# Optimization experiments

Measured on AMD Instinct MI355X. Metric: run time of the kernel, lower is better.

Reference implementation:

```python
import jax, jax.numpy as jnp
import numpy as np

H = 1024
B = 8
T = 2048

def setup_inputs() -> dict:
    key = jax.random.key(0)
    ks = jax.random.split(key, 12)
    s = 1.0 / np.sqrt(H)
    return {
        "x": jax.random.normal(ks[0], (B, T, H), dtype=jnp.float32),
        "time_decay": jax.random.normal(ks[1], (H,), dtype=jnp.float32) * 0.1,
        "time_first": jax.random.normal(ks[2], (H,), dtype=jnp.float32) * 0.1,
        "time_mix_key": jax.random.uniform(ks[3], (1, 1, H), dtype=jnp.float32),
        "time_mix_value": jax.random.uniform(ks[4], (1, 1, H), dtype=jnp.float32),
        "time_mix_receptance": jax.random.uniform(ks[5], (1, 1, H), dtype=jnp.float32),
        "Wk": jax.random.normal(ks[6], (H, H), dtype=jnp.float32) * s,
        "Wv": jax.random.normal(ks[7], (H, H), dtype=jnp.float32) * s,
        "Wr": jax.random.normal(ks[8], (H, H), dtype=jnp.float32) * s,
        "Wo": jax.random.normal(ks[9], (H, H), dtype=jnp.float32) * s,
        "bo": jax.random.normal(ks[10], (H,), dtype=jnp.float32) * 0.01,
    }

def reference(x, time_decay, time_first, time_mix_key, time_mix_value,
              time_mix_receptance, Wk, Wv, Wr, Wo, bo):
    # time shift: shifted[:, t] = x[:, t-1], shifted[:, 0] = 0
    shifted = jnp.pad(x, ((0, 0), (1, 0), (0, 0)))[:, :-1]
    k_in = x * time_mix_key + shifted * (1.0 - time_mix_key)
    v_in = x * time_mix_value + shifted * (1.0 - time_mix_value)
    r_in = x * time_mix_receptance + shifted * (1.0 - time_mix_receptance)
    k = jnp.einsum('bth,oh->bto', k_in, Wk)
    v = jnp.einsum('bth,oh->bto', v_in, Wv)
    r = jax.nn.sigmoid(jnp.einsum('bth,oh->bto', r_in, Wr))

    td = jnp.exp(-jnp.exp(time_decay))  # (H,)

    def step(carry, kv):
        num, den = carry            # (B, H) each
        k_t, v_t = kv               # (B, H) each
        e = jnp.exp(time_first + k_t)
        out_t = (num + e * v_t) / (den + e)
        ek = jnp.exp(k_t)
        return (td * num + ek * v_t, td * den + ek), out_t

    init = (jnp.zeros((x.shape[0], x.shape[2]), x.dtype),
            jnp.zeros((x.shape[0], x.shape[2]), x.dtype))
    # scan over time: (T, B, H)
    _, wkv = jax.lax.scan(step, init, (k.transpose(1, 0, 2), v.transpose(1, 0, 2)))
    wkv = wkv.transpose(1, 0, 2)    # (B, T, H)

    return jnp.einsum('bth,oh->bto', r * wkv, Wo) + bo
```

## Files before the change

kernel.cpp:

```cpp
#include <hip/hip_runtime.h>
#include <hip/hip_bf16.h>
#include <cstdint>
#include <cstddef>

#define HH 1024
#define BB 8
#define TT 2048
#define MM (BB*TT)
#define CC 128
#define LL (TT/CC)

typedef __attribute__((ext_vector_type(8))) short bf16x8;
typedef __attribute__((ext_vector_type(8))) unsigned short u16x8;
typedef __attribute__((ext_vector_type(4))) float f32x4;

__device__ __forceinline__ unsigned short f2bf(float f) {
  union { float f; unsigned u; } v; v.f = f;
  return (unsigned short)((v.u + 0x7fffu + ((v.u >> 16) & 1u)) >> 16);
}
__device__ __forceinline__ float bf2f(unsigned short s) {
  union { float f; unsigned u; } v; v.u = ((unsigned)s) << 16;
  return v.f;
}

__device__ __forceinline__ void load_lds16(const void* g, void* l) {
  __builtin_amdgcn_global_load_lds((const __attribute__((address_space(1))) void*)g,
                                   (__attribute__((address_space(3))) void*)l,
                                   16, 0, 0);
}

__global__ __launch_bounds__(256) void conv_w(const float* __restrict__ Wk,
    const float* __restrict__ Wv, const float* __restrict__ Wr,
    const float* __restrict__ Wo, unsigned short* __restrict__ dst) {
  const int i = (blockIdx.x * 256 + threadIdx.x) * 4;
  const float* src = blockIdx.y == 0 ? Wk : blockIdx.y == 1 ? Wv : blockIdx.y == 2 ? Wr : Wo;
  const float4 v = *(const float4*)(src + i);
  ushort4 o; o.x = f2bf(v.x); o.y = f2bf(v.y); o.z = f2bf(v.z); o.w = f2bf(v.w);
  *(ushort4*)(dst + (size_t)blockIdx.y * HH * HH + i) = o;
}

__global__ __launch_bounds__(256) void mix_kernel(const float* __restrict__ x,
    const float* __restrict__ tmk, const float* __restrict__ tmv, const float* __restrict__ tmr,
    unsigned short* __restrict__ kin, unsigned short* __restrict__ vin,
    unsigned short* __restrict__ rin) {
  const int gid = blockIdx.x * 256 + threadIdx.x;
  const size_t e0 = (size_t)gid * 4;
  const int h = (int)(e0 & (HH - 1));
  const int t = (int)((e0 >> 10) & (TT - 1));
  const float4 xv = *(const float4*)(x + e0);
  float4 sv = make_float4(0.f, 0.f, 0.f, 0.f);
  if (t != 0) sv = *(const float4*)(x + e0 - HH);
  const float4 k4 = *(const float4*)(tmk + h);
  const float4 v4 = *(const float4*)(tmv + h);
  const float4 r4 = *(const float4*)(tmr + h);
  ushort4 ko, vo, ro;
  ko.x = f2bf(sv.x + k4.x * (xv.x - sv.x)); ko.y = f2bf(sv.y + k4.y * (xv.y - sv.y));
  ko.z = f2bf(sv.z + k4.z * (xv.z - sv.z)); ko.w = f2bf(sv.w + k4.w * (xv.w - sv.w));
  vo.x = f2bf(sv.x + v4.x * (xv.x - sv.x)); vo.y = f2bf(sv.y + v4.y * (xv.y - sv.y));
  vo.z = f2bf(sv.z + v4.z * (xv.z - sv.z)); vo.w = f2bf(sv.w + v4.w * (xv.w - sv.w));
  ro.x = f2bf(sv.x + r4.x * (xv.x - sv.x)); ro.y = f2bf(sv.y + r4.y * (xv.y - sv.y));
  ro.z = f2bf(sv.z + r4.z * (xv.z - sv.z)); ro.w = f2bf(sv.w + r4.w * (xv.w - sv.w));
  *(ushort4*)(kin + e0) = ko;
  *(ushort4*)(vin + e0) = vo;
  *(ushort4*)(rin + e0) = ro;
}


#define BAR()   do { asm volatile("" ::: "memory"); __builtin_amdgcn_s_barrier(); \
                     asm volatile("" ::: "memory"); } while (0)
#define VM4()   asm volatile("s_waitcnt vmcnt(4)" ::: "memory")
#define VM0()   asm volatile("s_waitcnt vmcnt(0)" ::: "memory")
#define PRIO1() __builtin_amdgcn_s_setprio(1)
#define PRIO0() __builtin_amdgcn_s_setprio(0)

__device__ __forceinline__ void stA(const unsigned short* __restrict__ Ag, int m0, int kt,
                                    unsigned short* buf, int h, int w, int rl, int scol) {
#pragma unroll
  for (int l = 0; l < 2; ++l) {
    const int row = l * 128 + h * 64 + w * 8;
    load_lds16(Ag + (size_t)(m0 + row + rl) * HH + kt + scol, buf + row * 64);
  }
}
__device__ __forceinline__ void stB(const unsigned short* __restrict__ Bg, int n0, int kt,
                                    unsigned short* buf, int h, int w, int rl, int scol) {
#pragma unroll
  for (int l = 0; l < 2; ++l) {
    const int row = (2 * (l * 2 + (w >> 2)) + h) * 32 + (w & 3) * 8;
    load_lds16(Bg + (size_t)(n0 + row + rl) * HH + kt + scol, buf + row * 64);
  }
}

template<int MH>
__device__ __forceinline__ void rdA(const unsigned short* buf, bf16x8 (&af)[4][2],
                                    int wm, int l15, int kq, int swz) {
#pragma unroll
  for (int fm = 0; fm < 4; ++fm)
#pragma unroll
    for (int kk = 0; kk < 2; ++kk)
      af[fm][kk] = *(const bf16x8*)(buf + (wm * 128 + MH * 64 + fm * 16 + l15) * 64
                                        + ((kk * 32 + kq * 8) ^ swz));
}
__device__ __forceinline__ void rdBall(const unsigned short* buf, bf16x8 (&bfr)[2][2][2],
                                       int wn, int l15, int kq, int swz) {
#pragma unroll
  for (int nh = 0; nh < 2; ++nh)
#pragma unroll
    for (int fn = 0; fn < 2; ++fn)
#pragma unroll
      for (int kk = 0; kk < 2; ++kk)
        bfr[nh][fn][kk] = *(const bf16x8*)(buf + (wn * 64 + nh * 32 + fn * 16 + l15) * 64
                                               + ((kk * 32 + kq * 8) ^ swz));
}
template<int MH>
__device__ __forceinline__ void mfma32(f32x4 (&acc)[8][4], const bf16x8 (&af)[4][2],
                                       const bf16x8 (&bfr)[2][2][2]) {
#pragma unroll
  for (int nh = 0; nh < 2; ++nh)
#pragma unroll
    for (int fn = 0; fn < 2; ++fn)
#pragma unroll
      for (int kk = 0; kk < 2; ++kk)
#pragma unroll
        for (int fm = 0; fm < 4; ++fm)
          acc[MH * 4 + fm][nh * 2 + fn] = __builtin_amdgcn_mfma_f32_16x16x32_bf16(
              bfr[nh][fn][kk], af[fm][kk], acc[MH * 4 + fm][nh * 2 + fn], 0, 0, 0);
}

__device__ __forceinline__ void gemm256(const unsigned short* __restrict__ Ag,
                                        const unsigned short* __restrict__ Bg,
                                        const int m0, const int n0,
                                        unsigned short* As, unsigned short* Bs,
                                        f32x4 (&acc)[8][4]) {
  const int tid = threadIdx.x;
  const int lane = tid & 63;
  const int w = tid >> 6;
  const int wm = w >> 2, wn = w & 3;
  const int l15 = lane & 15, kq = lane >> 4;
  const int swz = (l15 & 7) << 3;
  const int rl = lane >> 3;
  const int scol = ((lane & 7) ^ rl) * 8;
  unsigned short* const A0 = As;
  unsigned short* const A1 = As + 256 * 64;
  unsigned short* const B0 = Bs;
  unsigned short* const B1 = Bs + 256 * 64;
  bf16x8 afA[4][2], afB[4][2], bfr[2][2][2];

  stA(Ag, m0, 0, A0, 0, w, rl, scol);
  stB(Bg, n0, 0, B0, 0, w, rl, scol);
  stB(Bg, n0, 0, B0, 1, w, rl, scol);
  stA(Ag, m0, 0, A0, 1, w, rl, scol);
  stA(Ag, m0, 64, A1, 0, w, rl, scol);
  stB(Bg, n0, 64, B1, 0, w, rl, scol);
  VM4();
  BAR();
  rdA<0>(A0, afA, wm, l15, kq, swz);
  rdBall(B0, bfr, wn, l15, kq, swz);

#pragma unroll 1
  for (int i = 0; i < 8; ++i) {
    const int t1  = ((2 * i + 1) * 64) & (HH - 1);
    const int tn0 = ((2 * i + 2) * 64) & (HH - 1);
    const int tn1 = ((2 * i + 3) * 64) & (HH - 1);

    BAR();
    stB(Bg, n0, t1, B1, 1, w, rl, scol);
    stA(Ag, m0, t1, A1, 1, w, rl, scol);
    rdA<1>(A0, afB, wm, l15, kq, swz);
    PRIO1(); mfma32<0>(acc, afA, bfr); PRIO0();

    VM0();
    BAR();
    stA(Ag, m0, tn0, A0, 0, w, rl, scol);
    stB(Bg, n0, tn0, B0, 0, w, rl, scol);
    rdA<0>(A1, afA, wm, l15, kq, swz);
    PRIO1(); mfma32<1>(acc, afB, bfr); PRIO0();
    rdBall(B1, bfr, wn, l15, kq, swz);

    BAR();
    stB(Bg, n0, tn0, B0, 1, w, rl, scol);
    stA(Ag, m0, tn0, A0, 1, w, rl, scol);
    rdA<1>(A1, afB, wm, l15, kq, swz);
    PRIO1(); mfma32<0>(acc, afA, bfr); PRIO0();

    VM0();
    BAR();
    stA(Ag, m0, tn1, A1, 0, w, rl, scol);
    stB(Bg, n0, tn1, B1, 0, w, rl, scol);
    rdA<0>(A0, afA, wm, l15, kq, swz);
    PRIO1(); mfma32<1>(acc, afB, bfr); PRIO0();
    rdBall(B0, bfr, wn, l15, kq, swz);
  }
  VM0();
}

__device__ __forceinline__ void swizzle_mn256(int x, int& m0, int& n0) {
  const int wg = (x & 7) * 32 + (x >> 3);
  m0 = (wg >> 2) * 256;
  n0 = (wg & 3) * 256;
}

__global__ __launch_bounds__(512, 2) void gemm_kvr(const unsigned short* __restrict__ kin,
    const unsigned short* __restrict__ vin, const unsigned short* __restrict__ rin,
    const unsigned short* __restrict__ Wbf,
    unsigned short* __restrict__ kb, unsigned short* __restrict__ vb,
    unsigned short* __restrict__ rb) {
  __shared__ unsigned short As[2 * 256 * 64];
  __shared__ unsigned short Bs[2 * 256 * 64];
  const int z = blockIdx.y;
  const unsigned short* Ag = z == 0 ? kin : (z == 1 ? vin : rin);
  const unsigned short* Bg = Wbf + (size_t)z * HH * HH;
  unsigned short* Cg = z == 0 ? kb : (z == 1 ? vb : rb);
  int m0, n0; swizzle_mn256(blockIdx.x, m0, n0);
  f32x4 acc[8][4] = {};
  gemm256(Ag, Bg, m0, n0, As, Bs, acc);
  const int lane = threadIdx.x & 63, w = threadIdx.x >> 6;
  const int wm = w >> 2, wn = w & 3, l15 = lane & 15, lq = lane >> 4;
  const bool sig = (z == 2);
#pragma unroll
  for (int fm = 0; fm < 8; ++fm) {
    const size_t mrow = (size_t)(m0 + wm * 128 + fm * 16 + l15) * HH;
#pragma unroll
    for (int fn = 0; fn < 4; ++fn) {
      const int ncol = n0 + wn * 64 + fn * 16 + lq * 4;
      float v0 = acc[fm][fn][0], v1 = acc[fm][fn][1];
      float v2 = acc[fm][fn][2], v3 = acc[fm][fn][3];
      if (sig) {
        v0 = 1.0f / (1.0f + __expf(-v0)); v1 = 1.0f / (1.0f + __expf(-v1));
        v2 = 1.0f / (1.0f + __expf(-v2)); v3 = 1.0f / (1.0f + __expf(-v3));
      }
      ushort4 o; o.x = f2bf(v0); o.y = f2bf(v1); o.z = f2bf(v2); o.w = f2bf(v3);
      *(ushort4*)(Cg + mrow + ncol) = o;
    }
  }
}

__global__ __launch_bounds__(512, 2) void gemm_o(const unsigned short* __restrict__ Ag,
    const unsigned short* __restrict__ Bg, const float* __restrict__ bias,
    float* __restrict__ C) {
  __shared__ unsigned short As[2 * 256 * 64];
  __shared__ unsigned short Bs[2 * 256 * 64];
  int m0, n0; swizzle_mn256(blockIdx.x, m0, n0);
  f32x4 acc[8][4] = {};
  gemm256(Ag, Bg, m0, n0, As, Bs, acc);
  const int lane = threadIdx.x & 63, w = threadIdx.x >> 6;
  const int wm = w >> 2, wn = w & 3, l15 = lane & 15, lq = lane >> 4;
#pragma unroll
  for (int fm = 0; fm < 8; ++fm) {
    const size_t mrow = (size_t)(m0 + wm * 128 + fm * 16 + l15) * HH;
#pragma unroll
    for (int fn = 0; fn < 4; ++fn) {
      const int ncol = n0 + wn * 64 + fn * 16 + lq * 4;
      const float4 bv = *(const float4*)(bias + ncol);
      float4 ov;
      ov.x = acc[fm][fn][0] + bv.x; ov.y = acc[fm][fn][1] + bv.y;
      ov.z = acc[fm][fn][2] + bv.z; ov.w = acc[fm][fn][3] + bv.w;
      *(float4*)(C + mrow + ncol) = ov;
    }
  }
}

__global__ __launch_bounds__(256) void wkv_part(const unsigned short* __restrict__ k,
    const unsigned short* __restrict__ v, const float* __restrict__ tdec,
    float* __restrict__ pnum, float* __restrict__ pden) {
  const int gid = blockIdx.x * 256 + threadIdx.x;
  const int h0 = (gid & 127) * 8;
  const int b = (gid >> 7) & (BB - 1);
  const int c = gid >> 10;
  float td[8], num[8], den[8];
#pragma unroll
  for (int j = 0; j < 8; ++j) {
    td[j] = __expf(-__expf(tdec[h0 + j]));
    num[j] = 0.f; den[j] = 0.f;
  }
  size_t idx = (size_t)b * TT * HH + (size_t)(c * LL) * HH + h0;
#pragma unroll 4
  for (int i = 0; i < LL; ++i, idx += HH) {
    const u16x8 k8 = *(const u16x8*)(k + idx);
    const u16x8 v8 = *(const u16x8*)(v + idx);
#pragma unroll
    for (int j = 0; j < 8; ++j) {
      const float ek = __expf(bf2f(k8[j]));
      num[j] = td[j] * num[j] + ek * bf2f(v8[j]);
      den[j] = td[j] * den[j] + ek;
    }
  }
  const size_t o = (size_t)c * (BB * HH) + b * HH + h0;
#pragma unroll
  for (int j = 0; j < 8; ++j) { pnum[o + j] = num[j]; pden[o + j] = den[j]; }
}

__global__ __launch_bounds__(256) void wkv_scan(const float* __restrict__ tdec,
    float* __restrict__ pnum, float* __restrict__ pden) {
  const int bh = blockIdx.x * 256 + threadIdx.x;
  const int h = bh & (HH - 1);
  const float ed = __expf(tdec[h]);
  const float tdL = __expf(-ed * (float)LL);
  float num = 0.f, den = 0.f;
#pragma unroll 8
  for (int c = 0; c < CC; ++c) {
    const size_t o = (size_t)c * (BB * HH) + bh;
    const float tn = pnum[o], td_ = pden[o];
    pnum[o] = num; pden[o] = den;
    num = tdL * num + tn;
    den = tdL * den + td_;
  }
}

__global__ __launch_bounds__(256) void wkv_final(const unsigned short* __restrict__ k,
    const unsigned short* __restrict__ v, const unsigned short* __restrict__ r,
    const float* __restrict__ tdec, const float* __restrict__ tfst,
    const float* __restrict__ pnum, const float* __restrict__ pden,
    unsigned short* __restrict__ rwkv) {
  const int gid = blockIdx.x * 256 + threadIdx.x;
  const int h0 = (gid & 127) * 8;
  const int b = (gid >> 7) & (BB - 1);
  const int c = gid >> 10;
  float td[8], etf[8], num[8], den[8];
  const size_t o = (size_t)c * (BB * HH) + b * HH + h0;
#pragma unroll
  for (int j = 0; j < 8; ++j) {
    td[j] = __expf(-__expf(tdec[h0 + j]));
    etf[j] = __expf(tfst[h0 + j]);
    num[j] = pnum[o + j]; den[j] = pden[o + j];
  }
  size_t idx = (size_t)b * TT * HH + (size_t)(c * LL) * HH + h0;
#pragma unroll 2
  for (int i = 0; i < LL; ++i, idx += HH) {
    const u16x8 k8 = *(const u16x8*)(k + idx);
    const u16x8 v8 = *(const u16x8*)(v + idx);
    const u16x8 r8 = *(const u16x8*)(r + idx);
    u16x8 o8;
#pragma unroll
    for (int j = 0; j < 8; ++j) {
      const float ek = __expf(bf2f(k8[j]));
      const float vt = bf2f(v8[j]);
      const float rt = bf2f(r8[j]);
      const float e = ek * etf[j];
      const float inv = __builtin_amdgcn_rcpf(den[j] + e);
      const float outv = (num[j] + e * vt) * inv;
      num[j] = td[j] * num[j] + ek * vt;
      den[j] = td[j] * den[j] + ek;
      o8[j] = f2bf(outv * rt);
    }
    *(u16x8*)(rwkv + idx) = o8;
  }
}

extern "C" void kernel_launch(void* const* d_in, const int* in_sizes, int n_in,
                              void* d_out, int out_size, void* d_ws, size_t ws_size,
                              hipStream_t stream) {
  (void)in_sizes; (void)n_in; (void)out_size; (void)ws_size;
  const float* x    = (const float*)d_in[0];
  const float* tdec = (const float*)d_in[1];
  const float* tfst = (const float*)d_in[2];
  const float* tmk  = (const float*)d_in[3];
  const float* tmv  = (const float*)d_in[4];
  const float* tmr  = (const float*)d_in[5];
  const float* Wk   = (const float*)d_in[6];
  const float* Wv   = (const float*)d_in[7];
  const float* Wr   = (const float*)d_in[8];
  const float* Wo   = (const float*)d_in[9];
  const float* bo   = (const float*)d_in[10];
  float* out = (float*)d_out;

  char* ws = (char*)d_ws;
  const size_t MiB = (size_t)1 << 20;
  unsigned short* Wbf = (unsigned short*)(ws);
  unsigned short* kin = (unsigned short*)(ws + 8 * MiB);
  unsigned short* vin = (unsigned short*)(ws + 40 * MiB);
  unsigned short* rin = (unsigned short*)(ws + 72 * MiB);
  unsigned short* rb  = (unsigned short*)(ws + 104 * MiB);
  unsigned short* kb = (unsigned short*)out;
  unsigned short* vb = kb + (size_t)MM * HH;
  unsigned short* rwkv = kin;
  float* pnum = (float*)(ws + 40 * MiB);
  float* pden = (float*)(ws + 44 * MiB);

  hipLaunchKernelGGL(conv_w, dim3(1024, 4), dim3(256), 0, stream, Wk, Wv, Wr, Wo, Wbf);
  hipLaunchKernelGGL(mix_kernel, dim3(16384), dim3(256), 0, stream,
                     x, tmk, tmv, tmr, kin, vin, rin);
  hipLaunchKernelGGL(gemm_kvr, dim3(256, 3), dim3(512), 0, stream,
                     kin, vin, rin, Wbf, kb, vb, rb);
  hipLaunchKernelGGL(wkv_part, dim3(512), dim3(256), 0, stream,
                     kb, vb, tdec, pnum, pden);
  hipLaunchKernelGGL(wkv_scan, dim3(32), dim3(256), 0, stream,
                     tdec, pnum, pden);
  hipLaunchKernelGGL(wkv_final, dim3(512), dim3(256), 0, stream,
                     kb, vb, rb, tdec, tfst, pnum, pden, rwkv);
  hipLaunchKernelGGL(gemm_o, dim3(256), dim3(512), 0, stream,
                     rwkv, Wbf + (size_t)3 * HH * HH, bo, out);
}
```

Baseline: 431.9 us.

## Switch GEMM core to 32x32x16 MFMA with restructured LDS pipeline

Replaces the 16x16x32 bf16 MFMA tiling with 32x32x16 MFMA fragments, cutting LDS fragment reads per MFMA flop. It also rewrites the main loop schedule: each 64-wide K tile is processed in four K=16 sub-steps, each with its own fragment reads and barriers, and global-to-LDS prefetch is reorganized. The new schedule adds many more barriers and removes the early prefetch of the second tile, which may expose load latency.

```diff
diff --git a/kernel.cpp b/kernel.cpp
--- a/kernel.cpp
+++ b/kernel.cpp
@@ -12,7 +12,7 @@
 
 typedef __attribute__((ext_vector_type(8))) short bf16x8;
 typedef __attribute__((ext_vector_type(8))) unsigned short u16x8;
-typedef __attribute__((ext_vector_type(4))) float f32x4;
+typedef __attribute__((ext_vector_type(16))) float f32x16;
 
 __device__ __forceinline__ unsigned short f2bf(float f) {
   union { float f; unsigned u; } v; v.f = f;
@@ -68,7 +68,6 @@
 
 #define BAR()   do { asm volatile("" ::: "memory"); __builtin_amdgcn_s_barrier(); \
                      asm volatile("" ::: "memory"); } while (0)
-#define VM4()   asm volatile("s_waitcnt vmcnt(4)" ::: "memory")
 #define VM0()   asm volatile("s_waitcnt vmcnt(0)" ::: "memory")
 #define PRIO1() __builtin_amdgcn_s_setprio(1)
 #define PRIO0() __builtin_amdgcn_s_setprio(0)
@@ -90,105 +89,82 @@
   }
 }
 
-template<int MH>
-__device__ __forceinline__ void rdA(const unsigned short* buf, bf16x8 (&af)[4][2],
-                                    int wm, int l15, int kq, int swz) {
-#pragma unroll
-  for (int fm = 0; fm < 4; ++fm)
-#pragma unroll
-    for (int kk = 0; kk < 2; ++kk)
-      af[fm][kk] = *(const bf16x8*)(buf + (wm * 128 + MH * 64 + fm * 16 + l15) * 64
-                                        + ((kk * 32 + kq * 8) ^ swz));
-}
-__device__ __forceinline__ void rdBall(const unsigned short* buf, bf16x8 (&bfr)[2][2][2],
-                                       int wn, int l15, int kq, int swz) {
-#pragma unroll
-  for (int nh = 0; nh < 2; ++nh)
-#pragma unroll
-    for (int fn = 0; fn < 2; ++fn)
-#pragma unroll
-      for (int kk = 0; kk < 2; ++kk)
-        bfr[nh][fn][kk] = *(const bf16x8*)(buf + (wn * 64 + nh * 32 + fn * 16 + l15) * 64
-                                               + ((kk * 32 + kq * 8) ^ swz));
-}
-template<int MH>
-__device__ __forceinline__ void mfma32(f32x4 (&acc)[8][4], const bf16x8 (&af)[4][2],
-                                       const bf16x8 (&bfr)[2][2][2]) {
-#pragma unroll
-  for (int nh = 0; nh < 2; ++nh)
-#pragma unroll
-    for (int fn = 0; fn < 2; ++fn)
-#pragma unroll
-      for (int kk = 0; kk < 2; ++kk)
-#pragma unroll
-        for (int fm = 0; fm < 4; ++fm)
-          acc[MH * 4 + fm][nh * 2 + fn] = __builtin_amdgcn_mfma_f32_16x16x32_bf16(
-              bfr[nh][fn][kk], af[fm][kk], acc[MH * 4 + fm][nh * 2 + fn], 0, 0, 0);
+__device__ __forceinline__ bf16x8 rd1(const unsigned short* buf, int row, int kq, int swz) {
+  return *(const bf16x8*)(buf + row * 64 + ((kq * 8) ^ swz));
+}
+__device__ __forceinline__ void rdS(const unsigned short* bA, const unsigned short* bB,
+                                    int wm, int wn, int l31, int kq, int swz,
+                                    bf16x8 (&af)[4], bf16x8 (&bfr)[2]) {
+  bfr[0] = rd1(bB, wn * 64 + l31, kq, swz);
+  af[0]  = rd1(bA, wm * 128 + l31, kq, swz);
+  bfr[1] = rd1(bB, wn * 64 + 32 + l31, kq, swz);
+  af[1]  = rd1(bA, wm * 128 + 32 + l31, kq, swz);
+  af[2]  = rd1(bA, wm * 128 + 64 + l31, kq, swz);
+  af[3]  = rd1(bA, wm * 128 + 96 + l31, kq, swz);
+}
+__device__ __forceinline__ void mfmaS(f32x16 (&acc)[4][2], const bf16x8 (&af)[4],
+                                      const bf16x8 (&bfr)[2]) {
+#pragma unroll
+  for (int mi = 0; mi < 4; ++mi)
+#pragma unroll
+    for (int nj = 0; nj < 2; ++nj)
+      acc[mi][nj] = __builtin_amdgcn_mfma_f32_32x32x16_bf16(bfr[nj], af[mi],
+                                                            acc[mi][nj], 0, 0, 0);
 }
 
 __device__ __forceinline__ void gemm256(const unsigned short* __restrict__ Ag,
                                         const unsigned short* __restrict__ Bg,
                                         const int m0, const int n0,
                                         unsigned short* As, unsigned short* Bs,
-                                        f32x4 (&acc)[8][4]) {
+                                        f32x16 (&acc)[4][2]) {
   const int tid = threadIdx.x;
   const int lane = tid & 63;
   const int w = tid >> 6;
   const int wm = w >> 2, wn = w & 3;
-  const int l15 = lane & 15, kq = lane >> 4;
-  const int swz = (l15 & 7) << 3;
+  const int l31 = lane & 31, lh = lane >> 5;
+  const int swz = (lane & 7) << 3;
   const int rl = lane >> 3;
   const int scol = ((lane & 7) ^ rl) * 8;
   unsigned short* const A0 = As;
   unsigned short* const A1 = As + 256 * 64;
   unsigned short* const B0 = Bs;
   unsigned short* const B1 = Bs + 256 * 64;
-  bf16x8 afA[4][2], afB[4][2], bfr[2][2][2];
+  bf16x8 af[4], bfr[2];
 
   stA(Ag, m0, 0, A0, 0, w, rl, scol);
+  stA(Ag, m0, 0, A0, 1, w, rl, scol);
   stB(Bg, n0, 0, B0, 0, w, rl, scol);
   stB(Bg, n0, 0, B0, 1, w, rl, scol);
-  stA(Ag, m0, 0, A0, 1, w, rl, scol);
-  stA(Ag, m0, 64, A1, 0, w, rl, scol);
-  stB(Bg, n0, 64, B1, 0, w, rl, scol);
-  VM4();
-  BAR();
-  rdA<0>(A0, afA, wm, l15, kq, swz);
-  rdBall(B0, bfr, wn, l15, kq, swz);
+  VM0(); BAR();
 
 #pragma unroll 1
   for (int i = 0; i < 8; ++i) {
     const int t1  = ((2 * i + 1) * 64) & (HH - 1);
     const int tn0 = ((2 * i + 2) * 64) & (HH - 1);
-    const int tn1 = ((2 * i + 3) * 64) & (HH - 1);
-
-    BAR();
+    rdS(A0, B0, wm, wn, l31, 0 + lh, swz, af, bfr);
+    stA(Ag, m0, t1, A1, 0, w, rl, scol);
+    stA(Ag, m0, t1, A1, 1, w, rl, scol);
+    BAR(); PRIO1(); mfmaS(acc, af, bfr); PRIO0(); BAR();
+    rdS(A0, B0, wm, wn, l31, 2 + lh, swz, af, bfr);
+    stB(Bg, n0, t1, B1, 0, w, rl, scol);
     stB(Bg, n0, t1, B1, 1, w, rl, scol);
-    stA(Ag, m0, t1, A1, 1, w, rl, scol);
-    rdA<1>(A0, afB, wm, l15, kq, swz);
-    PRIO1(); mfma32<0>(acc, afA, bfr); PRIO0();
-
-    VM0();
-    BAR();
+    BAR(); PRIO1(); mfmaS(acc, af, bfr); PRIO0(); BAR();
+    rdS(A0, B0, wm, wn, l31, 4 + lh, swz, af, bfr);
+    BAR(); PRIO1(); mfmaS(acc, af, bfr); PRIO0(); BAR();
+    rdS(A0, B0, wm, wn, l31, 6 + lh, swz, af, bfr);
+    BAR(); PRIO1(); mfmaS(acc, af, bfr); PRIO0(); VM0(); BAR();
+    rdS(A1, B1, wm, wn, l31, 0 + lh, swz, af, bfr);
     stA(Ag, m0, tn0, A0, 0, w, rl, scol);
+    stA(Ag, m0, tn0, A0, 1, w, rl, scol);
+    BAR(); PRIO1(); mfmaS(acc, af, bfr); PRIO0(); BAR();
+    rdS(A1, B1, wm, wn, l31, 2 + lh, swz, af, bfr);
     stB(Bg, n0, tn0, B0, 0, w, rl, scol);
-    rdA<0>(A1, afA, wm, l15, kq, swz);
-    PRIO1(); mfma32<1>(acc, afB, bfr); PRIO0();
-    rdBall(B1, bfr, wn, l15, kq, swz);
-
-    BAR();
     stB(Bg, n0, tn0, B0, 1, w, rl, scol);
-    stA(Ag, m0, tn0, A0, 1, w, rl, scol);
-    rdA<1>(A1, afB, wm, l15, kq, swz);
-    PRIO1(); mfma32<0>(acc, afA, bfr); PRIO0();
-
-    VM0();
-    BAR();
-    stA(Ag, m0, tn1, A1, 0, w, rl, scol);
-    stB(Bg, n0, tn1, B1, 0, w, rl, scol);
-    rdA<0>(A0, afA, wm, l15, kq, swz);
-    PRIO1(); mfma32<1>(acc, afB, bfr); PRIO0();
-    rdBall(B0, bfr, wn, l15, kq, swz);
+    BAR(); PRIO1(); mfmaS(acc, af, bfr); PRIO0(); BAR();
+    rdS(A1, B1, wm, wn, l31, 4 + lh, swz, af, bfr);
+    BAR(); PRIO1(); mfmaS(acc, af, bfr); PRIO0(); BAR();
+    rdS(A1, B1, wm, wn, l31, 6 + lh, swz, af, bfr);
+    BAR(); PRIO1(); mfmaS(acc, af, bfr); PRIO0(); VM0(); BAR();
   }
   VM0();
 }
@@ -211,25 +187,28 @@
   const unsigned short* Bg = Wbf + (size_t)z * HH * HH;
   unsigned short* Cg = z == 0 ? kb : (z == 1 ? vb : rb);
   int m0, n0; swizzle_mn256(blockIdx.x, m0, n0);
-  f32x4 acc[8][4] = {};
+  f32x16 acc[4][2] = {};
   gemm256(Ag, Bg, m0, n0, As, Bs, acc);
   const int lane = threadIdx.x & 63, w = threadIdx.x >> 6;
-  const int wm = w >> 2, wn = w & 3, l15 = lane & 15, lq = lane >> 4;
+  const int wm = w >> 2, wn = w & 3, l31 = lane & 31, lh = lane >> 5;
   const bool sig = (z == 2);
 #pragma unroll
-  for (int fm = 0; fm < 8; ++fm) {
-    const size_t mrow = (size_t)(m0 + wm * 128 + fm * 16 + l15) * HH;
-#pragma unroll
-    for (int fn = 0; fn < 4; ++fn) {
-      const int ncol = n0 + wn * 64 + fn * 16 + lq * 4;
-      float v0 = acc[fm][fn][0], v1 = acc[fm][fn][1];
-      float v2 = acc[fm][fn][2], v3 = acc[fm][fn][3];
-      if (sig) {
-        v0 = 1.0f / (1.0f + __expf(-v0)); v1 = 1.0f / (1.0f + __expf(-v1));
-        v2 = 1.0f / (1.0f + __expf(-v2)); v3 = 1.0f / (1.0f + __expf(-v3));
+  for (int mi = 0; mi < 4; ++mi) {
+    const size_t mrow = (size_t)(m0 + wm * 128 + mi * 32 + l31) * HH;
+#pragma unroll
+    for (int nj = 0; nj < 2; ++nj) {
+#pragma unroll
+      for (int g = 0; g < 4; ++g) {
+        const int ncol = n0 + wn * 64 + nj * 32 + 8 * g + 4 * lh;
+        float v0 = acc[mi][nj][g * 4 + 0], v1 = acc[mi][nj][g * 4 + 1];
+        float v2 = acc[mi][nj][g * 4 + 2], v3 = acc[mi][nj][g * 4 + 3];
+        if (sig) {
+          v0 = 1.0f / (1.0f + __expf(-v0)); v1 = 1.0f / (1.0f + __expf(-v1));
+          v2 = 1.0f / (1.0f + __expf(-v2)); v3 = 1.0f / (1.0f + __expf(-v3));
+        }
+        ushort4 o; o.x = f2bf(v0); o.y = f2bf(v1); o.z = f2bf(v2); o.w = f2bf(v3);
+        *(ushort4*)(Cg + mrow + ncol) = o;
       }
-      ushort4 o; o.x = f2bf(v0); o.y = f2bf(v1); o.z = f2bf(v2); o.w = f2bf(v3);
-      *(ushort4*)(Cg + mrow + ncol) = o;
     }
   }
 }
@@ -240,21 +219,24 @@
   __shared__ unsigned short As[2 * 256 * 64];
   __shared__ unsigned short Bs[2 * 256 * 64];
   int m0, n0; swizzle_mn256(blockIdx.x, m0, n0);
-  f32x4 acc[8][4] = {};
+  f32x16 acc[4][2] = {};
   gemm256(Ag, Bg, m0, n0, As, Bs, acc);
   const int lane = threadIdx.x & 63, w = threadIdx.x >> 6;
-  const int wm = w >> 2, wn = w & 3, l15 = lane & 15, lq = lane >> 4;
-#pragma unroll
-  for (int fm = 0; fm < 8; ++fm) {
-    const size_t mrow = (size_t)(m0 + wm * 128 + fm * 16 + l15) * HH;
-#pragma unroll
-    for (int fn = 0; fn < 4; ++fn) {
-      const int ncol = n0 + wn * 64 + fn * 16 + lq * 4;
-      const float4 bv = *(const float4*)(bias + ncol);
-      float4 ov;
-      ov.x = acc[fm][fn][0] + bv.x; ov.y = acc[fm][fn][1] + bv.y;
-      ov.z = acc[fm][fn][2] + bv.z; ov.w = acc[fm][fn][3] + bv.w;
-      *(float4*)(C + mrow + ncol) = ov;
+  const int wm = w >> 2, wn = w & 3, l31 = lane & 31, lh = lane >> 5;
+#pragma unroll
+  for (int mi = 0; mi < 4; ++mi) {
+    const size_t mrow = (size_t)(m0 + wm * 128 + mi * 32 + l31) * HH;
+#pragma unroll
+    for (int nj = 0; nj < 2; ++nj) {
+#pragma unroll
+      for (int g = 0; g < 4; ++g) {
+        const int ncol = n0 + wn * 64 + nj * 32 + 8 * g + 4 * lh;
+        const float4 bv = *(const float4*)(bias + ncol);
+        float4 ov;
+        ov.x = acc[mi][nj][g * 4 + 0] + bv.x; ov.y = acc[mi][nj][g * 4 + 1] + bv.y;
+        ov.z = acc[mi][nj][g * 4 + 2] + bv.z; ov.w = acc[mi][nj][g * 4 + 3] + bv.w;
+        *(float4*)(C + mrow + ncol) = ov;
+      }
     }
   }
 }
```

After: 379.6 us. 12.1% less time.
